# Performance work log

Hardware: AMD Instinct MI355X
Metric: run time of the kernel (lower is better)

The kernel has to match this reference:

```python
import jax, jax.numpy as jnp
import numpy as np

N = 50000      # nodes
E = 800000     # edges (before self loops)
IN = 256       # in_dim
HID = 32       # hidden_dim per head
H = 8          # heads layer 1
OUT = 64       # out_dim (classes)
NEG_SLOPE = 0.2  # PyG GATConv default


def gat_conv(x, ei, W, a_src, a_dst, b, heads, ch, concat):
    """PyG GATConv (eval mode, self-loops already in ei).
    x: [n, f_in], ei: [2, e] (row0=src j, row1=dst i), W: [f_in, heads*ch],
    a_src/a_dst: [heads, ch], b: [heads*ch] or [ch]."""
    n = x.shape[0]
    h = (x @ W).reshape(n, heads, ch)                      # [n, H, C]
    src, dst = ei[0], ei[1]
    alpha_src = (h * a_src).sum(-1)                        # [n, H]
    alpha_dst = (h * a_dst).sum(-1)                        # [n, H]
    e = jax.nn.leaky_relu(alpha_src[src] + alpha_dst[dst], NEG_SLOPE)  # [e, H]
    # segment softmax over incoming edges of each dst node
    emax = jax.lax.stop_gradient(jax.ops.segment_max(e, dst, num_segments=n))
    p = jnp.exp(e - emax[dst])
    denom = jax.ops.segment_sum(p, dst, num_segments=n)    # [n, H] (>0: self loops)
    alpha = p / denom[dst]                                 # [e, H]
    out = jax.ops.segment_sum(h[src] * alpha[:, :, None], dst, num_segments=n)  # [n, H, C]
    out = out.reshape(n, heads * ch) if concat else out.mean(axis=1)
    return out + b


def setup_inputs() -> dict:
    key = jax.random.key(0)
    ks = jax.random.split(key, 9)
    x = jax.random.normal(ks[0], (N, IN), jnp.float32)
    edge_index = jax.random.randint(ks[1], (2, E), 0, N, jnp.int32)
    W1 = jax.random.normal(ks[2], (IN, H * HID), jnp.float32) * 0.05
    a_src1 = jax.random.normal(ks[3], (H, HID), jnp.float32) * 0.1
    a_dst1 = jax.random.normal(ks[4], (H, HID), jnp.float32) * 0.1
    b1 = jnp.zeros((H * HID,), jnp.float32)
    W2 = jax.random.normal(ks[5], (H * HID, OUT), jnp.float32) * 0.05
    a_src2 = jax.random.normal(ks[6], (1, OUT), jnp.float32) * 0.1
    a_dst2 = jax.random.normal(ks[7], (1, OUT), jnp.float32) * 0.1
    b2 = jnp.zeros((OUT,), jnp.float32)
    return {"x": x, "edge_index": edge_index, "W1": W1, "a_src1": a_src1,
            "a_dst1": a_dst1, "b1": b1, "W2": W2, "a_src2": a_src2,
            "a_dst2": a_dst2, "b2": b2}


def reference(x, edge_index, W1, a_src1, a_dst1, b1, W2, a_src2, a_dst2, b2):
    n = x.shape[0]
    loops = jnp.arange(n, dtype=edge_index.dtype)
    ei = jnp.concatenate([edge_index, jnp.stack([loops, loops])], axis=1)  # add self loops
    h = gat_conv(x, ei, W1, a_src1, a_dst1, b1, H, HID, concat=True)
    h = jax.nn.relu(h)
    h = gat_conv(h, ei, W2, a_src2, a_dst2, b2, 1, OUT, concat=False)
    return jax.nn.log_softmax(h, axis=1)
```

## Files before the change

### kernel.cpp

```cpp
#include <hip/hip_runtime.h>
#include <math.h>

#define NNODES 50000
#define EORIG  800000
#define ETOT   850000
#define NBUCK  196
#define BSTRIDE 5120
#define P2CHUNK 4096
#define NBLK2  ((ETOT + P2CHUNK - 1)/P2CHUNK)

typedef __attribute__((ext_vector_type(8))) short bf8_t;
typedef __attribute__((ext_vector_type(4))) float f4_t;
typedef __attribute__((ext_vector_type(2))) float f2_t;

constexpr float LOG2E = 1.44269504f;

constexpr size_t align256(size_t x){ return (x + 255) & ~size_t(255); }
constexpr size_t OFF_OFFSETS = 0;
constexpr size_t OFF_DEG     = OFF_OFFSETS + align256((size_t)NNODES*4);
constexpr size_t OFF_GCUR    = OFF_DEG     + align256((size_t)NNODES*4);
constexpr size_t OFF_EPACK   = OFF_GCUR    + align256(NBUCK*4);
constexpr size_t OFF_SRC     = OFF_EPACK   + align256((size_t)NBUCK*BSTRIDE*4);
constexpr size_t OFF_AS1     = OFF_SRC     + align256((size_t)NBUCK*BSTRIDE*4);
constexpr size_t OFF_AD1     = OFF_AS1     + align256((size_t)NNODES*8*4);
constexpr size_t OFF_W1T     = OFF_AD1     + align256((size_t)NNODES*8*4);
constexpr size_t OFF_W2T     = OFF_W1T     + align256(256*256*2);
constexpr size_t OFF_H1F8    = OFF_W2T     + align256(64*256*2);
constexpr size_t OFF_OUT1B   = OFF_H1F8    + align256((size_t)NNODES*256);
constexpr size_t OFF_H2B     = OFF_H1F8;
constexpr size_t OFF_AS2     = OFF_OUT1B   + align256((size_t)NNODES*256*2);
constexpr size_t OFF_AD2     = OFF_AS2     + align256((size_t)NNODES*4);

__device__ __forceinline__ unsigned short f2bf(float f){
    union { float f; unsigned u; } v; v.f = f;
    unsigned r = v.u + 0x7FFF + ((v.u >> 16) & 1);
    return (unsigned short)(r >> 16);
}
__device__ __forceinline__ float bf2f(unsigned short s){
    union { unsigned u; float f; } v; v.u = ((unsigned)s) << 16;
    return v.f;
}


__global__ __launch_bounds__(256) void p3_part(const int* __restrict__ ei, int* __restrict__ gcur,
                                               int* __restrict__ epack){
    __shared__ int h[NBUCK];
    __shared__ int r[NBUCK];
    const int t = threadIdx.x;
    for (int i = t; i < NBUCK; i += 256){ h[i] = 0; r[i] = 0; }
    __syncthreads();
    const int base = blockIdx.x * P2CHUNK;
    int srcs[P2CHUNK/256], dsts[P2CHUNK/256];
#pragma unroll
    for (int j = 0; j < P2CHUNK/256; j++){
        int e = base + j*256 + t;
        if (e < ETOT){
            if (e < EORIG){ srcs[j] = ei[e]; dsts[j] = ei[EORIG + e]; }
            else          { srcs[j] = dsts[j] = e - EORIG; }
            atomicAdd(&h[dsts[j] >> 8], 1);
        } else dsts[j] = -1;
    }
    __syncthreads();
    for (int i = t; i < NBUCK; i += 256){
        int c = h[i];
        h[i] = c ? atomicAdd(&gcur[i], c) : 0;
    }
    __syncthreads();
#pragma unroll
    for (int j = 0; j < P2CHUNK/256; j++){
        if (dsts[j] >= 0){
            int b = dsts[j] >> 8;
            int rk = atomicAdd(&r[b], 1);
            epack[h[b] + rk] = (srcs[j] << 8) | (dsts[j] & 255);
        }
    }
}

__global__ __launch_bounds__(256) void p4_csr(const int* __restrict__ gcur, const int* __restrict__ epack,
                                              int* __restrict__ offsets, int* __restrict__ deg_g,
                                              int* __restrict__ srclist){
    __shared__ int deg[256];
    __shared__ int sm[256];
    __shared__ int cur[256];
    const int b = blockIdx.x, t = threadIdx.x;
    const int s0 = b * BSTRIDE, s1 = gcur[b];
    deg[t] = 0; __syncthreads();
    for (int i = s0 + t; i < s1; i += 256) atomicAdd(&deg[epack[i] & 255], 1);
    __syncthreads();
    int v = deg[t];
    sm[t] = v; __syncthreads();
    for (int off = 1; off < 256; off <<= 1){
        int add = (t >= off) ? sm[t-off] : 0;
        __syncthreads();
        sm[t] += add;
        __syncthreads();
    }
    int excl = sm[t] - v;
    int node = (b << 8) + t;
    if (node < NNODES){ offsets[node] = s0 + excl; deg_g[node] = v; }
    cur[t] = s0 + excl;
    __syncthreads();
    for (int i = s0 + t; i < s1; i += 256){
        int p = epack[i];
        int pos = atomicAdd(&cur[p & 255], 1);
        srclist[pos] = p >> 8;
    }
}


__global__ __launch_bounds__(256) void conv_w_k(const float* __restrict__ W1, const float* __restrict__ W2,
                                                short* __restrict__ w1t, short* __restrict__ w2t,
                                                int* __restrict__ gcur){
    int o = blockIdx.x*256 + threadIdx.x;
    if (o < NBUCK) gcur[o] = o * BSTRIDE;
    if (o < 256*256){
        int n = o >> 8, k = o & 255;
        w1t[o] = (short)f2bf(W1[k*256 + n]);
    } else {
        int o2 = o - 256*256;
        if (o2 < 64*256){
            int n = o2 >> 8, k = o2 & 255;
            w2t[o2] = (short)f2bf(W2[k*64 + n]);
        }
    }
}


__global__ __launch_bounds__(512) void gemm1_mfma(const float* __restrict__ x, const short* __restrict__ w1t,
        const float* __restrict__ a1s, const float* __restrict__ a1d,
        unsigned char* __restrict__ h1f8, float* __restrict__ as1, float* __restrict__ ad1){
    __shared__ short As[128][40];
    __shared__ short Bs[256][40];
    const int t = threadIdx.x;
    const int lane = t & 63, wave = t >> 6;
    const int wy = wave >> 2, wx = wave & 3;
    const int quad = lane >> 4, l15 = lane & 15;
    const int r0 = blockIdx.x * 128;
    const int srow = t >> 2, skoff = (t & 3) * 8;
    f4_t zero4 = {0.f,0.f,0.f,0.f};
    f4_t acc[4][4];
#pragma unroll
    for (int i=0;i<4;i++)
#pragma unroll
      for (int j=0;j<4;j++) acc[i][j] = zero4;

    for (int kk = 0; kk < 256; kk += 32){
        float4 xa0 = {0,0,0,0}, xa1 = {0,0,0,0};
        if (r0 + srow < NNODES){
            xa0 = *(const float4*)(x + (size_t)(r0+srow)*256 + kk + skoff);
            xa1 = *(const float4*)(x + (size_t)(r0+srow)*256 + kk + skoff + 4);
        }
        bf8_t b0  = *(const bf8_t*)(w1t + (size_t)(srow      )*256 + kk + skoff);
        bf8_t b1v = *(const bf8_t*)(w1t + (size_t)(srow + 128)*256 + kk + skoff);
        bf8_t a0;
        a0[0]=f2bf(xa0.x); a0[1]=f2bf(xa0.y); a0[2]=f2bf(xa0.z); a0[3]=f2bf(xa0.w);
        a0[4]=f2bf(xa1.x); a0[5]=f2bf(xa1.y); a0[6]=f2bf(xa1.z); a0[7]=f2bf(xa1.w);
        __syncthreads();
        *(bf8_t*)&As[srow     ][skoff] = a0;
        *(bf8_t*)&Bs[srow     ][skoff] = b0;
        *(bf8_t*)&Bs[srow+128][skoff] = b1v;
        __syncthreads();
        bf8_t af[4], bfr[4];
#pragma unroll
        for (int i=0;i<4;i++) af[i]  = *(const bf8_t*)&As[wy*64 + i*16 + l15][quad*8];
#pragma unroll
        for (int j=0;j<4;j++) bfr[j] = *(const bf8_t*)&Bs[wx*64 + j*16 + l15][quad*8];
#pragma unroll
        for (int i=0;i<4;i++)
#pragma unroll
          for (int j=0;j<4;j++)
            acc[i][j] = __builtin_amdgcn_mfma_f32_16x16x32_bf16(af[i], bfr[j], acc[i][j], 0,0,0);
    }
    const int colbase = wx*64;
    const int head0 = colbase >> 5;
    float cs[4], cd[4];
#pragma unroll
    for (int j=0;j<4;j++){
        cs[j] = a1s[colbase + j*16 + l15] * LOG2E;
        cd[j] = a1d[colbase + j*16 + l15] * LOG2E;
    }
#pragma unroll
    for (int i=0;i<4;i++){
        int rowb = r0 + wy*64 + i*16 + quad*4;
#pragma unroll
        for (int reg=0; reg<4; reg++){
            int row = rowb + reg;
            bool valid = row < NNODES;
            float sp0=0.f, dp0=0.f, sp1=0.f, dp1=0.f;
#pragma unroll
            for (int j=0;j<4;j++){
                float v = acc[i][j][reg];
                if (j < 2){ sp0 += v*cs[j]; dp0 += v*cd[j]; }
                else      { sp1 += v*cs[j]; dp1 += v*cd[j]; }
                if (valid){
                    unsigned enc = (unsigned)__builtin_amdgcn_cvt_pk_fp8_f32(v, v, 0, false);
                    h1f8[(size_t)row*256 + colbase + j*16 + l15] = (unsigned char)(enc & 0xffu);
                }
            }
            sp0 += __shfl_xor(sp0,1); sp0 += __shfl_xor(sp0,2); sp0 += __shfl_xor(sp0,4); sp0 += __shfl_xor(sp0,8);
            dp0 += __shfl_xor(dp0,1); dp0 += __shfl_xor(dp0,2); dp0 += __shfl_xor(dp0,4); dp0 += __shfl_xor(dp0,8);
            sp1 += __shfl_xor(sp1,1); sp1 += __shfl_xor(sp1,2); sp1 += __shfl_xor(sp1,4); sp1 += __shfl_xor(sp1,8);
            dp1 += __shfl_xor(dp1,1); dp1 += __shfl_xor(dp1,2); dp1 += __shfl_xor(dp1,4); dp1 += __shfl_xor(dp1,8);
            if (valid && l15 == 0){
                as1[row*8 + head0    ] = sp0;
                ad1[row*8 + head0    ] = dp0;
                as1[row*8 + head0 + 1] = sp1;
                ad1[row*8 + head0 + 1] = dp1;
            }
        }
    }
}


__global__ __launch_bounds__(256) void gemm2_mfma(const short* __restrict__ ab, const short* __restrict__ w2t,
        const float* __restrict__ a2s, const float* __restrict__ a2d,
        short* __restrict__ h2b, float* __restrict__ as2, float* __restrict__ ad2){
    __shared__ short As[128][40];
    __shared__ short Bs[64][40];
    const int t = threadIdx.x;
    const int lane = t & 63, wave = t >> 6;
    const int quad = lane >> 4, l15 = lane & 15;
    const int r0 = blockIdx.x * 128;
    const int srow = t >> 2, skoff = (t & 3) * 8;
    f4_t zero4 = {0.f,0.f,0.f,0.f};
    f4_t acc[2][4];
#pragma unroll
    for (int i=0;i<2;i++)
#pragma unroll
      for (int j=0;j<4;j++) acc[i][j] = zero4;

    for (int kk = 0; kk < 256; kk += 32){
        bf8_t a0 = {}, a1v = {};
        if (r0 + srow < NNODES)      a0  = *(const bf8_t*)(ab + (size_t)(r0+srow)*256 + kk + skoff);
        if (r0 + srow + 64 < NNODES) a1v = *(const bf8_t*)(ab + (size_t)(r0+srow+64)*256 + kk + skoff);
        bf8_t b0 = *(const bf8_t*)(w2t + (size_t)srow*256 + kk + skoff);
        __syncthreads();
        *(bf8_t*)&As[srow   ][skoff] = a0;
        *(bf8_t*)&As[srow+64][skoff] = a1v;
        *(bf8_t*)&Bs[srow   ][skoff] = b0;
        __syncthreads();
        bf8_t af[2], bfr[4];
#pragma unroll
        for (int i=0;i<2;i++) af[i]  = *(const bf8_t*)&As[wave*32 + i*16 + l15][quad*8];
#pragma unroll
        for (int j=0;j<4;j++) bfr[j] = *(const bf8_t*)&Bs[j*16 + l15][quad*8];
#pragma unroll
        for (int i=0;i<2;i++)
#pragma unroll
          for (int j=0;j<4;j++)
            acc[i][j] = __builtin_amdgcn_mfma_f32_16x16x32_bf16(af[i], bfr[j], acc[i][j], 0,0,0);
    }
    float cs[4], cd[4];
#pragma unroll
    for (int j=0;j<4;j++){
        cs[j] = a2s[j*16 + l15] * LOG2E;
        cd[j] = a2d[j*16 + l15] * LOG2E;
    }
#pragma unroll
    for (int i=0;i<2;i++){
        int rowb = r0 + wave*32 + i*16 + quad*4;
#pragma unroll
        for (int reg=0; reg<4; reg++){
            int row = rowb + reg;
            bool valid = row < NNODES;
            float sp=0.f, dp=0.f;
#pragma unroll
            for (int j=0;j<4;j++){
                float v = acc[i][j][reg];
                sp += v*cs[j]; dp += v*cd[j];
                if (valid) h2b[(size_t)row*64 + j*16 + l15] = (short)f2bf(v);
            }
            sp += __shfl_xor(sp,1); sp += __shfl_xor(sp,2); sp += __shfl_xor(sp,4); sp += __shfl_xor(sp,8);
            dp += __shfl_xor(dp,1); dp += __shfl_xor(dp,2); dp += __shfl_xor(dp,4); dp += __shfl_xor(dp,8);
            if (valid && l15 == 0){ as2[row] = sp; ad2[row] = dp; }
        }
    }
}


__global__ __launch_bounds__(256) void aggregate1_k(const unsigned char* __restrict__ h1f8,
        const float* __restrict__ as1, const float* __restrict__ ad1,
        const int* __restrict__ offsets, const int* __restrict__ deg_g,
        const int* __restrict__ srclist,
        const float* __restrict__ b1, short* __restrict__ out1b){
    int d = blockIdx.x*4 + (threadIdx.x >> 6);
    int lane = threadIdx.x & 63;
    if (d >= NNODES) return;
    const int head_g = lane >> 3;
    const int head_p = lane & 7;
    const int ep     = lane >> 3;
    int start = offsets[d];
    int deg = deg_g[d];
    float ad_p = ad1[d*8 + head_p];
    float denom = 0.f;
    f2_t acc01 = {0.f,0.f}, acc23 = {0.f,0.f};
    for (int w = 0; w < deg; w += 64){
        int deg_w = min(64, deg - w);
        int s_reg = srclist[start + w + min(lane, deg_w-1)];
        int ngr = (deg_w + 7) >> 3;
        auto comp_p = [&](int g)->float{
            int ei = g*8 + ep;
            int s  = __shfl(s_reg, min(ei, deg_w-1));
            float e = as1[s*8 + head_p] + ad_p;
            e = fmaxf(0.2f*e, e);
            float p = exp2f(e);
            return (ei < deg_w) ? p : 0.f;
        };
        float p_reg = comp_p(0);
        for (int g = 0; g < ngr; g++){
            float p_cur = p_reg;
            if (g + 1 < ngr) p_reg = comp_p(g+1);
#pragma unroll
            for (int e = 0; e < 8; e++){
                float pe = __shfl(p_cur, e*8 + head_g);
                int   se = __shfl(s_reg, g*8 + e);
                unsigned wv = *(const unsigned*)(h1f8 + (size_t)se*256 + lane*4);
                f2_t lo = __builtin_amdgcn_cvt_pk_f32_fp8(wv, false);
                f2_t hi = __builtin_amdgcn_cvt_pk_f32_fp8(wv, true);
                acc01 += pe*lo;
                acc23 += pe*hi;
                denom += pe;
            }
        }
    }
    float inv = 1.f / denom;
    float4 bv = *(const float4*)(b1 + lane*4);
    ushort4 us;
    us.x = f2bf(fmaxf(acc01[0]*inv + bv.x, 0.f));
    us.y = f2bf(fmaxf(acc01[1]*inv + bv.y, 0.f));
    us.z = f2bf(fmaxf(acc23[0]*inv + bv.z, 0.f));
    us.w = f2bf(fmaxf(acc23[1]*inv + bv.w, 0.f));
    *(ushort4*)(out1b + (size_t)d*256 + lane*4) = us;
}

__global__ __launch_bounds__(256) void aggregate2_k(const unsigned short* __restrict__ h2b,
        const float* __restrict__ as2, const float* __restrict__ ad2,
        const int* __restrict__ offsets, const int* __restrict__ deg_g,
        const int* __restrict__ srclist,
        const float* __restrict__ b2, float* __restrict__ out){
    int d = blockIdx.x*4 + (threadIdx.x >> 6);
    int lane = threadIdx.x & 63;
    if (d >= NNODES) return;
    int start = offsets[d];
    int deg = deg_g[d];
    float ad_v = ad2[d];
    float denom = 0.f, acc = 0.f;
    for (int w = 0; w < deg; w += 64){
        int deg_w = min(64, deg - w);
        int s_reg = srclist[start + w + min(lane, deg_w-1)];
        float ev = as2[s_reg] + ad_v;
        ev = fmaxf(0.2f*ev, ev);
        float p_lane = (lane < deg_w) ? exp2f(ev) : 0.f;
        int ngr = (deg_w + 7) >> 3;
        for (int g = 0; g < ngr; g++){
#pragma unroll
            for (int e2 = 0; e2 < 8; e2++){
                int ee = g*8 + e2;
                float pe = __shfl(p_lane, ee);
                int   se = __shfl(s_reg, ee);
                float hv = bf2f(h2b[(size_t)se*64 + lane]);
                acc += pe*hv;
                denom += pe;
            }
        }
    }
    float v = acc/denom + b2[lane];
    float mx = v;
#pragma unroll
    for (int off = 1; off < 64; off <<= 1) mx = fmaxf(mx, __shfl_xor(mx, off));
    float ex = __expf(v - mx);
    float ss = ex;
#pragma unroll
    for (int off = 1; off < 64; off <<= 1) ss += __shfl_xor(ss, off);
    out[(size_t)d*64 + lane] = v - mx - __logf(ss);
}


extern "C" void kernel_launch(void* const* d_in, const int* in_sizes, int n_in,
                              void* d_out, int out_size, void* d_ws, size_t ws_size,
                              hipStream_t stream){
    const float* x      = (const float*)d_in[0];
    const int*   ei     = (const int*)  d_in[1];
    const float* W1     = (const float*)d_in[2];
    const float* a_src1 = (const float*)d_in[3];
    const float* a_dst1 = (const float*)d_in[4];
    const float* b1     = (const float*)d_in[5];
    const float* W2     = (const float*)d_in[6];
    const float* a_src2 = (const float*)d_in[7];
    const float* a_dst2 = (const float*)d_in[8];
    const float* b2     = (const float*)d_in[9];

    char* ws = (char*)d_ws;
    int*   offsets = (int*)  (ws + OFF_OFFSETS);
    int*   deg_g   = (int*)  (ws + OFF_DEG);
    int*   gcur    = (int*)  (ws + OFF_GCUR);
    int*   epack   = (int*)  (ws + OFF_EPACK);
    int*   srclist = (int*)  (ws + OFF_SRC);
    float* as1     = (float*)(ws + OFF_AS1);
    float* ad1     = (float*)(ws + OFF_AD1);
    short* w1t     = (short*)(ws + OFF_W1T);
    short* w2t     = (short*)(ws + OFF_W2T);
    unsigned char* h1f8 = (unsigned char*)(ws + OFF_H1F8);
    short* out1b   = (short*)(ws + OFF_OUT1B);
    short* h2b     = (short*)(ws + OFF_H2B);
    float* as2     = (float*)(ws + OFF_AS2);
    float* ad2     = (float*)(ws + OFF_AD2);

    conv_w_k<<<(256*256 + 64*256 + 255)/256, 256, 0, stream>>>(W1, W2, w1t, w2t, gcur);

    p3_part<<<NBLK2, 256, 0, stream>>>(ei, gcur, epack);
    p4_csr <<<NBUCK, 256, 0, stream>>>(gcur, epack, offsets, deg_g, srclist);

    gemm1_mfma<<<(NNODES+127)/128, 512, 0, stream>>>(x, w1t, a_src1, a_dst1, h1f8, as1, ad1);
    aggregate1_k<<<(NNODES+3)/4, 256, 0, stream>>>(h1f8, as1, ad1, offsets, deg_g, srclist, b1, out1b);

    gemm2_mfma<<<(NNODES+127)/128, 256, 0, stream>>>(out1b, w2t, a_src2, a_dst2, h2b, as2, ad2);
    aggregate2_k<<<(NNODES+3)/4, 256, 0, stream>>>((const unsigned short*)h2b, as2, ad2, offsets, deg_g, srclist, b2, (float*)d_out);
}
```

Baseline: 247.8 us.

## Widen gather loads in aggregation kernels and split edges across lane subgroups

```diff
diff --git a/kernel.cpp b/kernel.cpp
--- a/kernel.cpp
+++ b/kernel.cpp
@@ -286,14 +286,18 @@
     int d = blockIdx.x*4 + (threadIdx.x >> 6);
     int lane = threadIdx.x & 63;
     if (d >= NNODES) return;
-    const int head_g = lane >> 3;
+    const int sub    = lane >> 4;
+    const int c16    = lane & 15;
+    const int head_g = c16 >> 1;
     const int head_p = lane & 7;
     const int ep     = lane >> 3;
     int start = offsets[d];
     int deg = deg_g[d];
     float ad_p = ad1[d*8 + head_p];
     float denom = 0.f;
-    f2_t acc01 = {0.f,0.f}, acc23 = {0.f,0.f};
+    f2_t acc[8];
+#pragma unroll
+    for (int i=0;i<8;i++) acc[i] = (f2_t){0.f,0.f};
     for (int w = 0; w < deg; w += 64){
         int deg_w = min(64, deg - w);
         int s_reg = srclist[start + w + min(lane, deg_w-1)];
@@ -311,26 +315,59 @@
             float p_cur = p_reg;
             if (g + 1 < ngr) p_reg = comp_p(g+1);
 #pragma unroll
-            for (int e = 0; e < 8; e++){
-                float pe = __shfl(p_cur, e*8 + head_g);
-                int   se = __shfl(s_reg, g*8 + e);
-                unsigned wv = *(const unsigned*)(h1f8 + (size_t)se*256 + lane*4);
-                f2_t lo = __builtin_amdgcn_cvt_pk_f32_fp8(wv, false);
-                f2_t hi = __builtin_amdgcn_cvt_pk_f32_fp8(wv, true);
-                acc01 += pe*lo;
-                acc23 += pe*hi;
+            for (int q = 0; q < 2; q++){
+                int eq = q*4 + sub;
+                float pe = __shfl(p_cur, eq*8 + head_g);
+                int   se = __shfl(s_reg, g*8 + eq);
+                uint4 wv = *(const uint4*)(h1f8 + (size_t)se*256 + c16*16);
+                f2_t v;
+                v = __builtin_amdgcn_cvt_pk_f32_fp8(wv.x, false); acc[0] += pe*v;
+                v = __builtin_amdgcn_cvt_pk_f32_fp8(wv.x, true);  acc[1] += pe*v;
+                v = __builtin_amdgcn_cvt_pk_f32_fp8(wv.y, false); acc[2] += pe*v;
+                v = __builtin_amdgcn_cvt_pk_f32_fp8(wv.y, true);  acc[3] += pe*v;
+                v = __builtin_amdgcn_cvt_pk_f32_fp8(wv.z, false); acc[4] += pe*v;
+                v = __builtin_amdgcn_cvt_pk_f32_fp8(wv.z, true);  acc[5] += pe*v;
+                v = __builtin_amdgcn_cvt_pk_f32_fp8(wv.w, false); acc[6] += pe*v;
+                v = __builtin_amdgcn_cvt_pk_f32_fp8(wv.w, true);  acc[7] += pe*v;
                 denom += pe;
             }
         }
     }
-    float inv = 1.f / denom;
-    float4 bv = *(const float4*)(b1 + lane*4);
-    ushort4 us;
-    us.x = f2bf(fmaxf(acc01[0]*inv + bv.x, 0.f));
-    us.y = f2bf(fmaxf(acc01[1]*inv + bv.y, 0.f));
-    us.z = f2bf(fmaxf(acc23[0]*inv + bv.z, 0.f));
-    us.w = f2bf(fmaxf(acc23[1]*inv + bv.w, 0.f));
-    *(ushort4*)(out1b + (size_t)d*256 + lane*4) = us;
+#pragma unroll
+    for (int i=0;i<8;i++){
+        acc[i][0] += __shfl_xor(acc[i][0], 16);
+        acc[i][1] += __shfl_xor(acc[i][1], 16);
+        acc[i][0] += __shfl_xor(acc[i][0], 32);
+        acc[i][1] += __shfl_xor(acc[i][1], 32);
+    }
+    denom += __shfl_xor(denom, 16);
+    denom += __shfl_xor(denom, 32);
+    if (sub == 0){
+        float inv = 1.f / denom;
+        const float4 bv0 = *(const float4*)(b1 + c16*16);
+        const float4 bv1 = *(const float4*)(b1 + c16*16 + 4);
+        const float4 bv2 = *(const float4*)(b1 + c16*16 + 8);
+        const float4 bv3 = *(const float4*)(b1 + c16*16 + 12);
+        bf8_t r0, r1;
+        r0[0] = (short)f2bf(fmaxf(acc[0][0]*inv + bv0.x, 0.f));
+        r0[1] = (short)f2bf(fmaxf(acc[0][1]*inv + bv0.y, 0.f));
+        r0[2] = (short)f2bf(fmaxf(acc[1][0]*inv + bv0.z, 0.f));
+        r0[3] = (short)f2bf(fmaxf(acc[1][1]*inv + bv0.w, 0.f));
+        r0[4] = (short)f2bf(fmaxf(acc[2][0]*inv + bv1.x, 0.f));
+        r0[5] = (short)f2bf(fmaxf(acc[2][1]*inv + bv1.y, 0.f));
+        r0[6] = (short)f2bf(fmaxf(acc[3][0]*inv + bv1.z, 0.f));
+        r0[7] = (short)f2bf(fmaxf(acc[3][1]*inv + bv1.w, 0.f));
+        r1[0] = (short)f2bf(fmaxf(acc[4][0]*inv + bv2.x, 0.f));
+        r1[1] = (short)f2bf(fmaxf(acc[4][1]*inv + bv2.y, 0.f));
+        r1[2] = (short)f2bf(fmaxf(acc[5][0]*inv + bv2.z, 0.f));
+        r1[3] = (short)f2bf(fmaxf(acc[5][1]*inv + bv2.w, 0.f));
+        r1[4] = (short)f2bf(fmaxf(acc[6][0]*inv + bv3.x, 0.f));
+        r1[5] = (short)f2bf(fmaxf(acc[6][1]*inv + bv3.y, 0.f));
+        r1[6] = (short)f2bf(fmaxf(acc[7][0]*inv + bv3.z, 0.f));
+        r1[7] = (short)f2bf(fmaxf(acc[7][1]*inv + bv3.w, 0.f));
+        *(bf8_t*)(out1b + (size_t)d*256 + c16*16)     = r0;
+        *(bf8_t*)(out1b + (size_t)d*256 + c16*16 + 8) = r1;
+    }
 }
 
 __global__ __launch_bounds__(256) void aggregate2_k(const unsigned short* __restrict__ h2b,
@@ -341,10 +378,13 @@
     int d = blockIdx.x*4 + (threadIdx.x >> 6);
     int lane = threadIdx.x & 63;
     if (d >= NNODES) return;
+    const int sub = lane >> 3;
+    const int c8  = lane & 7;
     int start = offsets[d];
     int deg = deg_g[d];
     float ad_v = ad2[d];
-    float denom = 0.f, acc = 0.f;
+    float denom = 0.f;
+    float accv[8] = {0.f,0.f,0.f,0.f,0.f,0.f,0.f,0.f};
     for (int w = 0; w < deg; w += 64){
         int deg_w = min(64, deg - w);
         int s_reg = srclist[start + w + min(lane, deg_w-1)];
@@ -353,26 +393,48 @@
         float p_lane = (lane < deg_w) ? exp2f(ev) : 0.f;
         int ngr = (deg_w + 7) >> 3;
         for (int g = 0; g < ngr; g++){
-#pragma unroll
-            for (int e2 = 0; e2 < 8; e2++){
-                int ee = g*8 + e2;
-                float pe = __shfl(p_lane, ee);
-                int   se = __shfl(s_reg, ee);
-                float hv = bf2f(h2b[(size_t)se*64 + lane]);
-                acc += pe*hv;
-                denom += pe;
-            }
-        }
-    }
-    float v = acc/denom + b2[lane];
-    float mx = v;
-#pragma unroll
-    for (int off = 1; off < 64; off <<= 1) mx = fmaxf(mx, __shfl_xor(mx, off));
-    float ex = __expf(v - mx);
-    float ss = ex;
-#pragma unroll
-    for (int off = 1; off < 64; off <<= 1) ss += __shfl_xor(ss, off);
-    out[(size_t)d*64 + lane] = v - mx - __logf(ss);
+            int eq = g*8 + sub;
+            float pe = __shfl(p_lane, eq);
+            int   se = __shfl(s_reg, eq);
+            bf8_t hv = *(const bf8_t*)(h2b + (size_t)se*64 + c8*8);
+#pragma unroll
+            for (int k=0;k<8;k++) accv[k] += pe * bf2f((unsigned short)hv[k]);
+            denom += pe;
+        }
+    }
+#pragma unroll
+    for (int k=0;k<8;k++){
+        accv[k] += __shfl_xor(accv[k], 8);
+        accv[k] += __shfl_xor(accv[k], 16);
+        accv[k] += __shfl_xor(accv[k], 32);
+    }
+    denom += __shfl_xor(denom, 8);
+    denom += __shfl_xor(denom, 16);
+    denom += __shfl_xor(denom, 32);
+    float inv = 1.f / denom;
+    float v[8];
+    float mx = -1e30f;
+#pragma unroll
+    for (int k=0;k<8;k++){
+        v[k] = accv[k]*inv + b2[c8*8 + k];
+        mx = fmaxf(mx, v[k]);
+    }
+    mx = fmaxf(mx, __shfl_xor(mx, 1));
+    mx = fmaxf(mx, __shfl_xor(mx, 2));
+    mx = fmaxf(mx, __shfl_xor(mx, 4));
+    float ss = 0.f;
+#pragma unroll
+    for (int k=0;k<8;k++) ss += __expf(v[k] - mx);
+    ss += __shfl_xor(ss, 1);
+    ss += __shfl_xor(ss, 2);
+    ss += __shfl_xor(ss, 4);
+    if (sub == 0){
+        float lg = mx + __logf(ss);
+        float4 o0 = {v[0]-lg, v[1]-lg, v[2]-lg, v[3]-lg};
+        float4 o1 = {v[4]-lg, v[5]-lg, v[6]-lg, v[7]-lg};
+        *(float4*)(out + (size_t)d*64 + c8*8)     = o0;
+        *(float4*)(out + (size_t)d*64 + c8*8 + 4) = o1;
+    }
 }
 
 
```

Result: no change. 249.1 us (+0.5%).

## Double-buffer gemm1 A tile with register-resident W, vectorize aggregate2 gathers

Applied to the files above, without the earlier changes.

```diff
diff --git a/kernel.cpp b/kernel.cpp
--- a/kernel.cpp
+++ b/kernel.cpp
@@ -126,17 +126,18 @@
 }
 
 
-__global__ __launch_bounds__(512) void gemm1_mfma(const float* __restrict__ x, const short* __restrict__ w1t,
+__global__ __launch_bounds__(256) void gemm1_mfma(const float* __restrict__ x, const short* __restrict__ w1t,
         const float* __restrict__ a1s, const float* __restrict__ a1d,
         unsigned char* __restrict__ h1f8, float* __restrict__ as1, float* __restrict__ ad1){
-    __shared__ short As[128][40];
-    __shared__ short Bs[256][40];
+    __shared__ short As[2][64][40];
     const int t = threadIdx.x;
     const int lane = t & 63, wave = t >> 6;
-    const int wy = wave >> 2, wx = wave & 3;
     const int quad = lane >> 4, l15 = lane & 15;
-    const int r0 = blockIdx.x * 128;
+    const int r0 = blockIdx.x * 64;
     const int srow = t >> 2, skoff = (t & 3) * 8;
+    const bool arow_ok = (r0 + srow) < NNODES;
+    const float* xrow = x + (size_t)(r0 + srow)*256 + skoff;
+    const short* wbase = w1t + (size_t)(wave*64 + l15)*256 + quad*8;
     f4_t zero4 = {0.f,0.f,0.f,0.f};
     f4_t acc[4][4];
 #pragma unroll
@@ -144,34 +145,47 @@
 #pragma unroll
       for (int j=0;j<4;j++) acc[i][j] = zero4;
 
-    for (int kk = 0; kk < 256; kk += 32){
-        float4 xa0 = {0,0,0,0}, xa1 = {0,0,0,0};
-        if (r0 + srow < NNODES){
-            xa0 = *(const float4*)(x + (size_t)(r0+srow)*256 + kk + skoff);
-            xa1 = *(const float4*)(x + (size_t)(r0+srow)*256 + kk + skoff + 4);
-        }
-        bf8_t b0  = *(const bf8_t*)(w1t + (size_t)(srow      )*256 + kk + skoff);
-        bf8_t b1v = *(const bf8_t*)(w1t + (size_t)(srow + 128)*256 + kk + skoff);
+    float4 xa0 = {0,0,0,0}, xa1 = {0,0,0,0};
+    if (arow_ok){ xa0 = *(const float4*)(xrow); xa1 = *(const float4*)(xrow + 4); }
+    bf8_t bcur[4], bnxt[4];
+#pragma unroll
+    for (int j=0;j<4;j++) bcur[j] = *(const bf8_t*)(wbase + j*16*256);
+    {
         bf8_t a0;
         a0[0]=f2bf(xa0.x); a0[1]=f2bf(xa0.y); a0[2]=f2bf(xa0.z); a0[3]=f2bf(xa0.w);
         a0[4]=f2bf(xa1.x); a0[5]=f2bf(xa1.y); a0[6]=f2bf(xa1.z); a0[7]=f2bf(xa1.w);
-        __syncthreads();
-        *(bf8_t*)&As[srow     ][skoff] = a0;
-        *(bf8_t*)&Bs[srow     ][skoff] = b0;
-        *(bf8_t*)&Bs[srow+128][skoff] = b1v;
-        __syncthreads();
-        bf8_t af[4], bfr[4];
-#pragma unroll
-        for (int i=0;i<4;i++) af[i]  = *(const bf8_t*)&As[wy*64 + i*16 + l15][quad*8];
-#pragma unroll
-        for (int j=0;j<4;j++) bfr[j] = *(const bf8_t*)&Bs[wx*64 + j*16 + l15][quad*8];
+        *(bf8_t*)&As[0][srow][skoff] = a0;
+    }
+    __syncthreads();
+    int cur = 0;
+#pragma unroll
+    for (int s = 0; s < 8; s++){
+        if (s < 7){
+            const int kn = s*32 + 32;
+            if (arow_ok){ xa0 = *(const float4*)(xrow + kn); xa1 = *(const float4*)(xrow + kn + 4); }
+#pragma unroll
+            for (int j=0;j<4;j++) bnxt[j] = *(const bf8_t*)(wbase + j*16*256 + kn);
+        }
+        bf8_t af[4];
+#pragma unroll
+        for (int i=0;i<4;i++) af[i] = *(const bf8_t*)&As[cur][i*16 + l15][quad*8];
 #pragma unroll
         for (int i=0;i<4;i++)
 #pragma unroll
           for (int j=0;j<4;j++)
-            acc[i][j] = __builtin_amdgcn_mfma_f32_16x16x32_bf16(af[i], bfr[j], acc[i][j], 0,0,0);
-    }
-    const int colbase = wx*64;
+            acc[i][j] = __builtin_amdgcn_mfma_f32_16x16x32_bf16(af[i], bcur[j], acc[i][j], 0,0,0);
+        if (s < 7){
+            bf8_t a0;
+            a0[0]=f2bf(xa0.x); a0[1]=f2bf(xa0.y); a0[2]=f2bf(xa0.z); a0[3]=f2bf(xa0.w);
+            a0[4]=f2bf(xa1.x); a0[5]=f2bf(xa1.y); a0[6]=f2bf(xa1.z); a0[7]=f2bf(xa1.w);
+            *(bf8_t*)&As[cur^1][srow][skoff] = a0;
+            __syncthreads();
+            cur ^= 1;
+#pragma unroll
+            for (int j=0;j<4;j++) bcur[j] = bnxt[j];
+        }
+    }
+    const int colbase = wave*64;
     const int head0 = colbase >> 5;
     float cs[4], cd[4];
 #pragma unroll
@@ -181,7 +195,7 @@
     }
 #pragma unroll
     for (int i=0;i<4;i++){
-        int rowb = r0 + wy*64 + i*16 + quad*4;
+        int rowb = r0 + i*16 + quad*4;
 #pragma unroll
         for (int reg=0; reg<4; reg++){
             int row = rowb + reg;
@@ -341,10 +355,13 @@
     int d = blockIdx.x*4 + (threadIdx.x >> 6);
     int lane = threadIdx.x & 63;
     if (d >= NNODES) return;
+    const int sub = lane >> 3;
+    const int c8  = lane & 7;
     int start = offsets[d];
     int deg = deg_g[d];
     float ad_v = ad2[d];
-    float denom = 0.f, acc = 0.f;
+    float denom = 0.f;
+    float accv[8] = {0.f,0.f,0.f,0.f,0.f,0.f,0.f,0.f};
     for (int w = 0; w < deg; w += 64){
         int deg_w = min(64, deg - w);
         int s_reg = srclist[start + w + min(lane, deg_w-1)];
@@ -353,26 +370,48 @@
         float p_lane = (lane < deg_w) ? exp2f(ev) : 0.f;
         int ngr = (deg_w + 7) >> 3;
         for (int g = 0; g < ngr; g++){
-#pragma unroll
-            for (int e2 = 0; e2 < 8; e2++){
-                int ee = g*8 + e2;
-                float pe = __shfl(p_lane, ee);
-                int   se = __shfl(s_reg, ee);
-                float hv = bf2f(h2b[(size_t)se*64 + lane]);
-                acc += pe*hv;
-                denom += pe;
-            }
-        }
-    }
-    float v = acc/denom + b2[lane];
-    float mx = v;
-#pragma unroll
-    for (int off = 1; off < 64; off <<= 1) mx = fmaxf(mx, __shfl_xor(mx, off));
-    float ex = __expf(v - mx);
-    float ss = ex;
-#pragma unroll
-    for (int off = 1; off < 64; off <<= 1) ss += __shfl_xor(ss, off);
-    out[(size_t)d*64 + lane] = v - mx - __logf(ss);
+            int eq = g*8 + sub;
+            float pe = __shfl(p_lane, eq);
+            int   se = __shfl(s_reg, eq);
+            bf8_t hv = *(const bf8_t*)(h2b + (size_t)se*64 + c8*8);
+#pragma unroll
+            for (int k=0;k<8;k++) accv[k] += pe * bf2f((unsigned short)hv[k]);
+            denom += pe;
+        }
+    }
+#pragma unroll
+    for (int k=0;k<8;k++){
+        accv[k] += __shfl_xor(accv[k], 8);
+        accv[k] += __shfl_xor(accv[k], 16);
+        accv[k] += __shfl_xor(accv[k], 32);
+    }
+    denom += __shfl_xor(denom, 8);
+    denom += __shfl_xor(denom, 16);
+    denom += __shfl_xor(denom, 32);
+    float inv = 1.f / denom;
+    float v[8];
+    float mx = -1e30f;
+#pragma unroll
+    for (int k=0;k<8;k++){
+        v[k] = accv[k]*inv + b2[c8*8 + k];
+        mx = fmaxf(mx, v[k]);
+    }
+    mx = fmaxf(mx, __shfl_xor(mx, 1));
+    mx = fmaxf(mx, __shfl_xor(mx, 2));
+    mx = fmaxf(mx, __shfl_xor(mx, 4));
+    float ss = 0.f;
+#pragma unroll
+    for (int k=0;k<8;k++) ss += __expf(v[k] - mx);
+    ss += __shfl_xor(ss, 1);
+    ss += __shfl_xor(ss, 2);
+    ss += __shfl_xor(ss, 4);
+    if (sub == 0){
+        float lg = mx + __logf(ss);
+        float4 o0 = {v[0]-lg, v[1]-lg, v[2]-lg, v[3]-lg};
+        float4 o1 = {v[4]-lg, v[5]-lg, v[6]-lg, v[7]-lg};
+        *(float4*)(out + (size_t)d*64 + c8*8)     = o0;
+        *(float4*)(out + (size_t)d*64 + c8*8 + 4) = o1;
+    }
 }
 
 
@@ -411,7 +450,7 @@
     p3_part<<<NBLK2, 256, 0, stream>>>(ei, gcur, epack);
     p4_csr <<<NBUCK, 256, 0, stream>>>(gcur, epack, offsets, deg_g, srclist);
 
-    gemm1_mfma<<<(NNODES+127)/128, 512, 0, stream>>>(x, w1t, a_src1, a_dst1, h1f8, as1, ad1);
+    gemm1_mfma<<<(NNODES+63)/64, 256, 0, stream>>>(x, w1t, a_src1, a_dst1, h1f8, as1, ad1);
     aggregate1_k<<<(NNODES+3)/4, 256, 0, stream>>>(h1f8, as1, ad1, offsets, deg_g, srclist, b1, out1b);
 
     gemm2_mfma<<<(NNODES+127)/128, 256, 0, stream>>>(out1b, w2t, a_src2, a_dst2, h2b, as2, ad2);
```

Result: no change. 246.6 us (-0.5%).
